# Kernel optimization log

Measured on AMD Instinct MI355X. Metric: run time of the kernel, lower is better.

The kernel has to match this reference:

```python
import jax, jax.numpy as jnp
import numpy as np

N, C, V, T, M = 4, 64, 25, 300, 2
H, HD = 8, 32
E = H * HD  # 256

def setup_inputs() -> dict:
    key = jax.random.key(0)
    ks = jax.random.split(key, 6)
    x = jax.random.normal(ks[0], (N, C, V, T, M), dtype=jnp.float32)
    w_qkv = jax.random.normal(ks[1], (C, 3 * E), dtype=jnp.float32) * (C ** -0.5)
    b_qkv = jnp.zeros((3 * E,), dtype=jnp.float32)
    w_merge = jax.random.normal(ks[2], (E, C), dtype=jnp.float32) * (E ** -0.5)
    b_merge = jnp.zeros((C,), dtype=jnp.float32)
    bias_table = jax.random.normal(ks[3], (2 * T - 1, HD), dtype=jnp.float32) * 0.02
    return {"x": x, "w_qkv": w_qkv, "b_qkv": b_qkv, "w_merge": w_merge,
            "b_merge": b_merge, "bias_table": bias_table}

def reference(x, w_qkv, b_qkv, w_merge, b_merge, bias_table):
    n, c, v, t, m = x.shape
    scale = E ** (-0.5)
    xp = jnp.transpose(x, (0, 4, 2, 3, 1))          # N M V T C
    qkv = xp @ w_qkv + b_qkv                         # N M V T 3E
    q, k, val = jnp.split(qkv, 3, axis=-1)
    def to_heads(z):
        z = z.reshape(n * m, v, t, H, HD)
        return jnp.transpose(z, (0, 1, 3, 2, 4))     # B V H T HD
    q, k, val = to_heads(q), to_heads(k), to_heads(val)
    scores = jnp.einsum('bvhid,bvhjd->bvhij', q, k) * scale
    rel = jnp.arange(t)
    idx = rel[:, None] - rel[None, :] + (t - 1)      # T T
    pos_bias = bias_table[idx]                       # T T HD
    rel_scores = jnp.einsum('bvhld,lrd->bvhlr', q, pos_bias)
    attn = jax.nn.softmax(scores + rel_scores, axis=-1)
    out = jnp.einsum('bvhij,bvhjd->bvhid', attn, val)  # B V H T HD
    out = jnp.transpose(out, (0, 1, 3, 2, 4)).reshape(n, m, v, t, E)
    out = out @ w_merge + b_merge                    # N M V T C
    return jnp.transpose(out, (0, 4, 2, 3, 1))       # N C V T M
```

## Files before the change

### kernel.cpp

```cpp
#include <hip/hip_runtime.h>
#include <cstdint>

#define NN 4
#define CC 64
#define VV 25
#define TT 300
#define MM 2
#define HH 8
#define HD 32
#define EE 256

typedef short bf16x8 __attribute__((ext_vector_type(8)));
typedef float f32x4 __attribute__((ext_vector_type(4)));
typedef float f32x2 __attribute__((ext_vector_type(2)));
typedef unsigned int u32x4 __attribute__((ext_vector_type(4)));

__device__ __forceinline__ unsigned short f2bf(float f) {
  union { float f; unsigned u; } x; x.f = f;
  unsigned r = x.u + 0x7FFF + ((x.u >> 16) & 1);
  return (unsigned short)(r >> 16);
}
__device__ __forceinline__ float bf2f(unsigned short s) {
  union { unsigned u; float f; } x; x.u = ((unsigned)s) << 16;
  return x.f;
}
__device__ __forceinline__ unsigned short truncbf(float f) {
  union { float f; unsigned u; } x; x.f = f;
  return (unsigned short)(x.u >> 16);
}
__device__ __forceinline__ float bperm(int byteaddr, float v) {
  return __int_as_float(__builtin_amdgcn_ds_bpermute(byteaddr, __float_as_int(v)));
}
__device__ __forceinline__ void unpack8(u32x4 a, u32x4 b, bf16x8& H8, bf16x8& L8) {
  union { unsigned u[4]; bf16x8 v; } H, L;
  H.u[0] = (a[1] & 0xFFFF0000u) | (a[0] >> 16);
  H.u[1] = (a[3] & 0xFFFF0000u) | (a[2] >> 16);
  H.u[2] = (b[1] & 0xFFFF0000u) | (b[0] >> 16);
  H.u[3] = (b[3] & 0xFFFF0000u) | (b[2] >> 16);
  L.u[0] = (a[1] << 16) | (a[0] & 0xFFFFu);
  L.u[1] = (a[3] << 16) | (a[2] & 0xFFFFu);
  L.u[2] = (b[1] << 16) | (b[0] & 0xFFFFu);
  L.u[3] = (b[3] << 16) | (b[2] & 0xFFFFu);
  H8 = H.v; L8 = L.v;
}

#define QKN 15360000
#define VTN 16384000
#define LOG2E 1.4426950408889634f

__global__ __launch_bounds__(256) void prep_kernel(
    const float* __restrict__ w_qkv, const float* __restrict__ w_merge,
    const float* __restrict__ bias_table,
    unsigned short* __restrict__ WqTh, unsigned short* __restrict__ WqTl,
    unsigned short* __restrict__ WhT, unsigned short* __restrict__ WlT,
    unsigned short* __restrict__ btPad)
{
  int i = blockIdx.x * 256 + threadIdx.x;
  if (i < 49152) {
    int c = i / 768, e = i % 768;
    float v = w_qkv[i];
    unsigned short hb = truncbf(v);
    WqTh[e * 64 + c] = hb; WqTl[e * 64 + c] = f2bf(v - bf2f(hb));
  } else if (i < 65536) {
    int j = i - 49152;
    int e = j >> 6, c = j & 63;
    float v = w_merge[j];
    unsigned short hb = truncbf(v);
    WhT[c * EE + e] = hb; WlT[c * EE + e] = f2bf(v - bf2f(hb));
  } else if (i < 65536 + 22528) {
    int j = i - 65536;
    int row = j >> 5, d = j & 31;
    int g = row - 20;
    float v = (g >= 0 && g < 2 * TT - 1) ? bias_table[g * 32 + d] : 0.f;
    btPad[j] = f2bf(v);
  }
}

__global__ __launch_bounds__(256, 3) void qkv_kernel(
    const float* __restrict__ x, const float* __restrict__ b_qkv,
    const unsigned short* __restrict__ WqTh, const unsigned short* __restrict__ WqTl,
    unsigned* __restrict__ Qp,
    unsigned short* __restrict__ Kh, unsigned short* __restrict__ Kl,
    unsigned short* __restrict__ Vt)
{
  __shared__ __align__(16) union {
    unsigned int a[64 * 68];
    unsigned short vtr[256 * 66];
  } sm;

  int blk = blockIdx.x;
  int tt = blk % 5; blk /= 5;
  int v25 = blk % 25; int b = blk / 25;
  int n = b >> 1, m = b & 1;
  int t0 = tt * 60;
  int tid = threadIdx.x;
  int w = tid >> 6, lane = tid & 63, quad = lane >> 4, c16 = lane & 15;

  for (int i = tid; i < 64 * 64; i += 256) {
    int c = i >> 6, t = i & 63;
    float val = 0.f;
    if (t < 60) val = x[((((size_t)n * CC + c) * VV + v25) * TT + (t0 + t)) * MM + m];
    union { float f; unsigned u; } xb; xb.f = val;
    unsigned hi16 = xb.u & 0xFFFF0000u;
    unsigned short lb = f2bf(val - __uint_as_float(hi16));
    sm.a[t * 68 + c] = hi16 | (unsigned)lb;
  }
  __syncthreads();

  bf16x8 ah[4][2], al[4][2];
  #pragma unroll
  for (int mt = 0; mt < 4; ++mt)
    #pragma unroll
    for (int kc = 0; kc < 2; ++kc) {
      const u32x4* p = (const u32x4*)&sm.a[(mt * 16 + c16) * 68 + kc * 32 + quad * 8];
      unpack8(p[0], p[1], ah[mt][kc], al[mt][kc]);
    }
  __syncthreads();

  size_t bv = (size_t)(b * VV + v25);
  int e0w = w * 192;
  for (int nt = 0; nt < 12; ++nt) {
    int ebase = e0w + nt * 16;
    int e = ebase + c16;
    bf16x8 bh[2], bl[2];
    #pragma unroll
    for (int kc = 0; kc < 2; ++kc) {
      bh[kc] = *(const bf16x8*)&WqTh[(size_t)e * 64 + kc * 32 + quad * 8];
      bl[kc] = *(const bf16x8*)&WqTl[(size_t)e * 64 + kc * 32 + quad * 8];
    }
    f32x4 acc[4];
    #pragma unroll
    for (int mt = 0; mt < 4; ++mt) {
      acc[mt] = (f32x4){0.f, 0.f, 0.f, 0.f};
      #pragma unroll
      for (int kc = 0; kc < 2; ++kc) {
        acc[mt] = __builtin_amdgcn_mfma_f32_16x16x32_bf16(ah[mt][kc], bh[kc], acc[mt], 0, 0, 0);
        acc[mt] = __builtin_amdgcn_mfma_f32_16x16x32_bf16(al[mt][kc], bh[kc], acc[mt], 0, 0, 0);
        acc[mt] = __builtin_amdgcn_mfma_f32_16x16x32_bf16(ah[mt][kc], bl[kc], acc[mt], 0, 0, 0);
      }
    }
    float bias = b_qkv[e];
    int which = ebase >> 8;
    if (which == 0) {
      int hh = (e >> 5) & 7, dd = e & 31;
      size_t rowb = (bv * HH + hh) * TT;
      #pragma unroll
      for (int mt = 0; mt < 4; ++mt)
        #pragma unroll
        for (int reg = 0; reg < 4; ++reg) {
          int lrow = mt * 16 + quad * 4 + reg;
          if (lrow < 60) {
            int t = t0 + lrow;
            float s = (acc[mt][reg] + bias) * LOG2E;
            union { float f; unsigned u; } sb; sb.f = s;
            unsigned hi16 = sb.u & 0xFFFF0000u;
            unsigned short lb2 = f2bf(s - __uint_as_float(hi16));
            Qp[(rowb + t) * HD + dd] = hi16 | (unsigned)lb2;
          }
        }
    } else if (which == 1) {
      int hh = (e >> 5) & 7, dd = e & 31;
      size_t rowb = (bv * HH + hh) * TT;
      #pragma unroll
      for (int mt = 0; mt < 4; ++mt)
        #pragma unroll
        for (int reg = 0; reg < 4; ++reg) {
          int lrow = mt * 16 + quad * 4 + reg;
          if (lrow < 60) {
            int t = t0 + lrow;
            float s = (acc[mt][reg] + bias) * 0.0625f;
            unsigned short hb = truncbf(s);
            size_t idx = (rowb + t) * HD + dd;
            Kh[idx] = hb; Kl[idx] = f2bf(s - bf2f(hb));
          }
        }
    } else {
      int ep = e - 512;
      #pragma unroll
      for (int mt = 0; mt < 4; ++mt)
        #pragma unroll
        for (int reg = 0; reg < 4; ++reg)
          sm.vtr[ep * 66 + mt * 16 + quad * 4 + reg] = f2bf(acc[mt][reg] + bias);
    }
  }
  __syncthreads();
  for (int i = tid; i < 256 * 30; i += 256) {
    int ep = i / 30, tc = (i % 30) * 2;
    int e = 512 + ep;
    int hh = (e >> 5) & 7, dd = e & 31;
    size_t idx = ((bv * HH + hh) * HD + dd) * 320 + t0 + tc;
    *(unsigned int*)&Vt[idx] = *(const unsigned int*)&sm.vtr[ep * 66 + tc];
  }
}

__global__ __launch_bounds__(256, 3) void attn17_kernel(
    const unsigned* __restrict__ Qp,
    const unsigned short* __restrict__ Kh, const unsigned short* __restrict__ Kl,
    const unsigned short* __restrict__ Vt, const unsigned short* __restrict__ btPad,
    unsigned short* __restrict__ Oh, unsigned short* __restrict__ Ol)
{
  __shared__ __align__(16) unsigned short sPh[2][128 * 72];

  int bid0 = blockIdx.x;
  int bid = (bid0 & 7) * 600 + (bid0 >> 3);
  int lt = bid % 3; int rest = bid / 3;
  int h = rest & 7; rest >>= 3;
  int v = rest % 25; int b = rest / 25;
  int l0 = lt * 128;
  int tid = threadIdx.x;
  int w = tid >> 6, lane = tid & 63, quad = lane >> 4, c16 = lane & 15;
  if (l0 + 32 * w >= TT) return;
  size_t tbase = ((size_t)(b * VV + v) * HH + h) * TT;
  size_t vbase = ((size_t)(b * VV + v) * HH + h) * HD;

  const unsigned short* Qp16 = (const unsigned short*)Qp;
  bf16x8 qh[2], qlw[2];
  #pragma unroll
  for (int mt = 0; mt < 2; ++mt) {
    size_t qo = (tbase + l0 + w * 32 + mt * 16 + c16) * HD + quad * 8;
    bf16x8 raw0 = *(const bf16x8*)&Qp16[qo * 2];
    bf16x8 raw1 = *(const bf16x8*)&Qp16[qo * 2 + 8];
    union { bf16x8 v; u32x4 u; } A, B;
    A.v = raw0; B.v = raw1;
    unpack8(A.u, B.u, qh[mt], qlw[mt]);
  }

  int srcaddr[4]; bool sel[4];
  #pragma unroll
  for (int reg = 0; reg < 4; ++reg) {
    srcaddr[reg] = 4 * (quad * 16 + ((15 + 4 * quad + reg - c16) & 15));
    sel[reg] = (4 * quad + reg) > c16;
  }

  f32x4 accO[2][2];
  #pragma unroll
  for (int mt = 0; mt < 2; ++mt)
    #pragma unroll
    for (int no = 0; no < 2; ++no)
      accO[mt][no] = (f32x4){0.f, 0.f, 0.f, 0.f};
  float psum[2][4] = {{0.f, 0.f, 0.f, 0.f}, {0.f, 0.f, 0.f, 0.f}};

  #pragma unroll
  for (int rt = 0; rt < 5; ++rt) {
    const int r0 = rt * 64;
    unsigned short* myP = &sPh[rt & 1][32 * w * 72];

    const unsigned short* kb = &Kh[(tbase + r0 + c16) * HD + quad * 8];
    const unsigned short* lb = &Kl[(tbase + r0 + c16) * HD + quad * 8];
    bf16x8 khv[4], klv[4];
    #pragma unroll
    for (int nt = 0; nt < 4; ++nt) {
      khv[nt] = *(const bf16x8*)&kb[nt * 16 * HD];
      klv[nt] = *(const bf16x8*)&lb[nt * 16 * HD];
    }
    bf16x8 vv[2][2];
    if (rt > 0) {
      int p0 = r0 - 64;
      #pragma unroll
      for (int kc = 0; kc < 2; ++kc)
        #pragma unroll
        for (int no = 0; no < 2; ++no)
          vv[kc][no] = *(const bf16x8*)&Vt[(vbase + no * 16 + c16) * 320 + p0 + kc * 32 + quad * 8];
    }
    const unsigned short* btb = &btPad[(size_t)(l0 + 256 + 32 * w - r0 + c16) * HD + quad * 8];
    bf16x8 bt6[6];
    #pragma unroll
    for (int j = 0; j < 6; ++j) bt6[j] = *(const bf16x8*)&btb[j * 16 * HD];

    #pragma unroll
    for (int mt = 0; mt < 2; ++mt) {
      float BA[4], BB[4], BC[4] = {0.f, 0.f, 0.f, 0.f};
      {
        f32x4 r = {0.f, 0.f, 0.f, 0.f};
        r = __builtin_amdgcn_mfma_f32_16x16x32_bf16(qh[mt], bt6[mt + 4], r, 0, 0, 0);
        f32x4 r2 = {0.f, 0.f, 0.f, 0.f};
        r2 = __builtin_amdgcn_mfma_f32_16x16x32_bf16(qh[mt], bt6[mt + 3], r2, 0, 0, 0);
        #pragma unroll
        for (int reg = 0; reg < 4; ++reg) BA[reg] = bperm(srcaddr[reg], r[reg]);
        #pragma unroll
        for (int reg = 0; reg < 4; ++reg) BB[reg] = bperm(srcaddr[reg], r2[reg]);
      }
      #pragma unroll
      for (int nt = 0; nt < 4; ++nt) {
        f32x4 sc = {0.f, 0.f, 0.f, 0.f};
        sc = __builtin_amdgcn_mfma_f32_16x16x32_bf16(qh[mt],  khv[nt], sc, 0, 0, 0);
        sc = __builtin_amdgcn_mfma_f32_16x16x32_bf16(qlw[mt], khv[nt], sc, 0, 0, 0);
        sc = __builtin_amdgcn_mfma_f32_16x16x32_bf16(qh[mt],  klv[nt], sc, 0, 0, 0);
        if (nt < 3) {
          f32x4 r = {0.f, 0.f, 0.f, 0.f};
          r = __builtin_amdgcn_mfma_f32_16x16x32_bf16(qh[mt], bt6[mt + 2 - nt], r, 0, 0, 0);
          #pragma unroll
          for (int reg = 0; reg < 4; ++reg) BC[reg] = bperm(srcaddr[reg], r[reg]);
        }

        bool bad = (r0 + nt * 16 + c16) >= TT;
        #pragma unroll
        for (int reg = 0; reg < 4; ++reg) {
          float ri = sel[reg] ? BA[reg] : BB[reg];
          float p = bad ? 0.f : __builtin_amdgcn_exp2f(sc[reg] + ri);
          psum[mt][reg] += p;
          myP[(mt * 16 + 4 * quad + reg) * 72 + nt * 16 + c16] = f2bf(p);
        }
        #pragma unroll
        for (int reg = 0; reg < 4; ++reg) { BA[reg] = BB[reg]; BB[reg] = BC[reg]; }
      }
    }

    if (rt > 0) {
      unsigned short* prevP = &sPh[(rt - 1) & 1][32 * w * 72];
      #pragma unroll
      for (int mt = 0; mt < 2; ++mt)
        #pragma unroll
        for (int kc = 0; kc < 2; ++kc) {
          bf16x8 pf = *(const bf16x8*)&prevP[(mt * 16 + c16) * 72 + kc * 32 + quad * 8];
          #pragma unroll
          for (int no = 0; no < 2; ++no)
            accO[mt][no] = __builtin_amdgcn_mfma_f32_16x16x32_bf16(pf, vv[kc][no], accO[mt][no], 0, 0, 0);
        }
    }
  }
  {
    int p0 = 4 * 64;
    unsigned short* prevP = &sPh[0][32 * w * 72];
    #pragma unroll
    for (int kc = 0; kc < 2; ++kc) {
      bf16x8 vfr[2];
      #pragma unroll
      for (int no = 0; no < 2; ++no)
        vfr[no] = *(const bf16x8*)&Vt[(vbase + no * 16 + c16) * 320 + p0 + kc * 32 + quad * 8];
      #pragma unroll
      for (int mt = 0; mt < 2; ++mt) {
        bf16x8 pf = *(const bf16x8*)&prevP[(mt * 16 + c16) * 72 + kc * 32 + quad * 8];
        #pragma unroll
        for (int no = 0; no < 2; ++no)
          accO[mt][no] = __builtin_amdgcn_mfma_f32_16x16x32_bf16(pf, vfr[no], accO[mt][no], 0, 0, 0);
      }
    }
  }

  #pragma unroll
  for (int mt = 0; mt < 2; ++mt)
    #pragma unroll
    for (int reg = 0; reg < 4; ++reg) {
      #pragma unroll
      for (int off = 1; off <= 8; off <<= 1)
        psum[mt][reg] += __shfl_xor(psum[mt][reg], off);
    }
  size_t obase = (size_t)(b * VV + v) * TT;
  #pragma unroll
  for (int mt = 0; mt < 2; ++mt)
    #pragma unroll
    for (int no = 0; no < 2; ++no)
      #pragma unroll
      for (int reg = 0; reg < 4; ++reg) {
        int gl = l0 + 32 * w + 16 * mt + 4 * quad + reg;
        if (gl < TT) {
          float o = accO[mt][no][reg] / psum[mt][reg];
          size_t oi = (obase + gl) * EE + h * HD + no * 16 + c16;
          unsigned short hb = truncbf(o);
          Oh[oi] = hb; Ol[oi] = f2bf(o - bf2f(hb));
        }
      }
}

__global__ __launch_bounds__(256, 4) void merge4_kernel(
    const unsigned short* __restrict__ Oh, const unsigned short* __restrict__ Ol,
    const unsigned short* __restrict__ WhT, const unsigned short* __restrict__ WlT,
    const float* __restrict__ b_merge, float* __restrict__ out)
{
  int blk = blockIdx.x;
  int tt = blk % 10; blk /= 10;
  int v = blk % 25; int nb = blk / 25;
  int tid = threadIdx.x;
  int w = tid >> 6, lane = tid & 63, quad = lane >> 4, c16 = lane & 15;
  int t0 = tt * 30;
  int cidx = w * 16 + c16;
  size_t obase0 = ((size_t)(nb * 2 + 0) * VV + v) * TT;
  size_t obase1 = ((size_t)(nb * 2 + 1) * VV + v) * TT;

  f32x4 acc[2][2];
  #pragma unroll
  for (int mm = 0; mm < 2; ++mm)
    #pragma unroll
    for (int mt = 0; mt < 2; ++mt)
      acc[mm][mt] = (f32x4){0.f, 0.f, 0.f, 0.f};

  for (int ks = 0; ks < 8; ++ks) {
    int eoff = ks * 32 + quad * 8;
    bf16x8 bh = *(const bf16x8*)&WhT[(size_t)cidx * EE + eoff];
    bf16x8 bl = *(const bf16x8*)&WlT[(size_t)cidx * EE + eoff];
    #pragma unroll
    for (int mm = 0; mm < 2; ++mm) {
      size_t ob = (mm == 0) ? obase0 : obase1;
      #pragma unroll
      for (int mt = 0; mt < 2; ++mt) {
        size_t ao = (ob + t0 + mt * 16 + c16) * EE + eoff;
        bf16x8 ahv = *(const bf16x8*)&Oh[ao];
        bf16x8 alv = *(const bf16x8*)&Ol[ao];
        acc[mm][mt] = __builtin_amdgcn_mfma_f32_16x16x32_bf16(ahv, bh, acc[mm][mt], 0, 0, 0);
        acc[mm][mt] = __builtin_amdgcn_mfma_f32_16x16x32_bf16(alv, bh, acc[mm][mt], 0, 0, 0);
        acc[mm][mt] = __builtin_amdgcn_mfma_f32_16x16x32_bf16(ahv, bl, acc[mm][mt], 0, 0, 0);
      }
    }
  }
  float bm = b_merge[cidx];
  size_t rowbase = ((size_t)nb * CC + cidx) * VV + v;
  #pragma unroll
  for (int mt = 0; mt < 2; ++mt)
    #pragma unroll
    for (int reg = 0; reg < 4; ++reg) {
      int lrow = mt * 16 + 4 * quad + reg;
      if (lrow < 30) {
        int t = t0 + lrow;
        f32x2 pr;
        pr[0] = acc[0][mt][reg] + bm;
        pr[1] = acc[1][mt][reg] + bm;
        *(f32x2*)&out[rowbase * TT * MM + (size_t)t * MM] = pr;
      }
    }
}

extern "C" void kernel_launch(void* const* d_in, const int* in_sizes, int n_in,
                              void* d_out, int out_size, void* d_ws, size_t ws_size,
                              hipStream_t stream) {
  const float* x          = (const float*)d_in[0];
  const float* w_qkv      = (const float*)d_in[1];
  const float* b_qkv      = (const float*)d_in[2];
  const float* w_merge    = (const float*)d_in[3];
  const float* b_merge    = (const float*)d_in[4];
  const float* bias_table = (const float*)d_in[5];
  float* out = (float*)d_out;
  unsigned short* ws16 = (unsigned short*)d_ws;
  unsigned* Qp = (unsigned*)ws16;
  unsigned short* Kh   = ws16 + (size_t)2 * QKN;
  unsigned short* Kl   = ws16 + (size_t)3 * QKN;
  unsigned short* Vt   = ws16 + (size_t)4 * QKN;
  unsigned short* Oh   = ws16 + (size_t)4 * QKN + VTN;
  unsigned short* Ol   = ws16 + (size_t)5 * QKN + VTN;
  unsigned short* base8 = ws16 + (size_t)6 * QKN + VTN;
  unsigned short* WhT  = base8;
  unsigned short* WlT  = base8 + 16384;
  unsigned short* WqTh = base8 + 32768;
  unsigned short* WqTl = base8 + 81920;
  unsigned short* btPad = base8 + 131072;

  prep_kernel<<<dim3(344), dim3(256), 0, stream>>>(w_qkv, w_merge, bias_table,
                                                   WqTh, WqTl, WhT, WlT, btPad);
  qkv_kernel<<<dim3(1000), dim3(256), 0, stream>>>(x, b_qkv, WqTh, WqTl,
                                                   Qp, Kh, Kl, Vt);
  attn17_kernel<<<dim3(4800), dim3(256), 0, stream>>>(Qp, Kh, Kl, Vt, btPad, Oh, Ol);
  merge4_kernel<<<dim3(1000), dim3(256), 0, stream>>>(Oh, Ol, WhT, WlT, b_merge, out);
}
```

Baseline: 296.0 us.

## Fuse attention and merge projection into one kernel looping over heads

The attention and merge kernels become one kernel. Each block now handles one (b, v, l-tile) and loops over all 8 heads. After each head it normalises the output, stages it in LDS as a hi/lo bf16 split, and accumulates that head's part of the merge GEMM in registers. This removes the Oh/Ol round-trip through global memory and one kernel launch. The cost is a grid cut from 4800 to 600 blocks, which reduces parallelism on a device with many CUs, and the final stores are scattered scalar writes.

```diff
diff --git a/kernel.cpp b/kernel.cpp
--- a/kernel.cpp
+++ b/kernel.cpp
@@ -193,37 +193,26 @@
   }
 }
 
-__global__ __launch_bounds__(256, 3) void attn17_kernel(
+__global__ __launch_bounds__(256, 3) void attn_merge_kernel(
     const unsigned* __restrict__ Qp,
     const unsigned short* __restrict__ Kh, const unsigned short* __restrict__ Kl,
     const unsigned short* __restrict__ Vt, const unsigned short* __restrict__ btPad,
-    unsigned short* __restrict__ Oh, unsigned short* __restrict__ Ol)
+    const unsigned short* __restrict__ WhT, const unsigned short* __restrict__ WlT,
+    const float* __restrict__ b_merge, float* __restrict__ out)
 {
   __shared__ __align__(16) unsigned short sPh[2][128 * 72];
+  __shared__ __align__(16) unsigned oLds[4 * 32 * 32];
 
   int bid0 = blockIdx.x;
-  int bid = (bid0 & 7) * 600 + (bid0 >> 3);
+  int bid = (bid0 & 7) * 75 + (bid0 >> 3);
   int lt = bid % 3; int rest = bid / 3;
-  int h = rest & 7; rest >>= 3;
   int v = rest % 25; int b = rest / 25;
   int l0 = lt * 128;
   int tid = threadIdx.x;
   int w = tid >> 6, lane = tid & 63, quad = lane >> 4, c16 = lane & 15;
   if (l0 + 32 * w >= TT) return;
-  size_t tbase = ((size_t)(b * VV + v) * HH + h) * TT;
-  size_t vbase = ((size_t)(b * VV + v) * HH + h) * HD;
 
   const unsigned short* Qp16 = (const unsigned short*)Qp;
-  bf16x8 qh[2], qlw[2];
-  #pragma unroll
-  for (int mt = 0; mt < 2; ++mt) {
-    size_t qo = (tbase + l0 + w * 32 + mt * 16 + c16) * HD + quad * 8;
-    bf16x8 raw0 = *(const bf16x8*)&Qp16[qo * 2];
-    bf16x8 raw1 = *(const bf16x8*)&Qp16[qo * 2 + 8];
-    union { bf16x8 v; u32x4 u; } A, B;
-    A.v = raw0; B.v = raw1;
-    unpack8(A.u, B.u, qh[mt], qlw[mt]);
-  }
 
   int srcaddr[4]; bool sel[4];
   #pragma unroll
@@ -232,192 +221,190 @@
     sel[reg] = (4 * quad + reg) > c16;
   }
 
-  f32x4 accO[2][2];
+  f32x4 oacc[2][4];
   #pragma unroll
   for (int mt = 0; mt < 2; ++mt)
     #pragma unroll
-    for (int no = 0; no < 2; ++no)
-      accO[mt][no] = (f32x4){0.f, 0.f, 0.f, 0.f};
-  float psum[2][4] = {{0.f, 0.f, 0.f, 0.f}, {0.f, 0.f, 0.f, 0.f}};
-
+    for (int ct = 0; ct < 4; ++ct)
+      oacc[mt][ct] = (f32x4){0.f, 0.f, 0.f, 0.f};
+
+  unsigned* oL = &oLds[w * 1024];
+
+  for (int h = 0; h < 8; ++h) {
+    size_t tbase = ((size_t)(b * VV + v) * HH + h) * TT;
+    size_t vbase = ((size_t)(b * VV + v) * HH + h) * HD;
+
+    bf16x8 qh[2], qlw[2];
+    #pragma unroll
+    for (int mt = 0; mt < 2; ++mt) {
+      size_t qo = (tbase + l0 + w * 32 + mt * 16 + c16) * HD + quad * 8;
+      bf16x8 raw0 = *(const bf16x8*)&Qp16[qo * 2];
+      bf16x8 raw1 = *(const bf16x8*)&Qp16[qo * 2 + 8];
+      union { bf16x8 v; u32x4 u; } A, B;
+      A.v = raw0; B.v = raw1;
+      unpack8(A.u, B.u, qh[mt], qlw[mt]);
+    }
+
+    f32x4 accO[2][2];
+    #pragma unroll
+    for (int mt = 0; mt < 2; ++mt)
+      #pragma unroll
+      for (int no = 0; no < 2; ++no)
+        accO[mt][no] = (f32x4){0.f, 0.f, 0.f, 0.f};
+    float psum[2][4] = {{0.f, 0.f, 0.f, 0.f}, {0.f, 0.f, 0.f, 0.f}};
+
+    #pragma unroll
+    for (int rt = 0; rt < 5; ++rt) {
+      const int r0 = rt * 64;
+      unsigned short* myP = &sPh[rt & 1][32 * w * 72];
+
+      const unsigned short* kb = &Kh[(tbase + r0 + c16) * HD + quad * 8];
+      const unsigned short* lb = &Kl[(tbase + r0 + c16) * HD + quad * 8];
+      bf16x8 khv[4], klv[4];
+      #pragma unroll
+      for (int nt = 0; nt < 4; ++nt) {
+        khv[nt] = *(const bf16x8*)&kb[nt * 16 * HD];
+        klv[nt] = *(const bf16x8*)&lb[nt * 16 * HD];
+      }
+      bf16x8 vv[2][2];
+      if (rt > 0) {
+        int p0 = r0 - 64;
+        #pragma unroll
+        for (int kc = 0; kc < 2; ++kc)
+          #pragma unroll
+          for (int no = 0; no < 2; ++no)
+            vv[kc][no] = *(const bf16x8*)&Vt[(vbase + no * 16 + c16) * 320 + p0 + kc * 32 + quad * 8];
+      }
+      const unsigned short* btb = &btPad[(size_t)(l0 + 256 + 32 * w - r0 + c16) * HD + quad * 8];
+      bf16x8 bt6[6];
+      #pragma unroll
+      for (int j = 0; j < 6; ++j) bt6[j] = *(const bf16x8*)&btb[j * 16 * HD];
+
+      #pragma unroll
+      for (int mt = 0; mt < 2; ++mt) {
+        float BA[4], BB[4], BC[4] = {0.f, 0.f, 0.f, 0.f};
+        {
+          f32x4 r = {0.f, 0.f, 0.f, 0.f};
+          r = __builtin_amdgcn_mfma_f32_16x16x32_bf16(qh[mt], bt6[mt + 4], r, 0, 0, 0);
+          f32x4 r2 = {0.f, 0.f, 0.f, 0.f};
+          r2 = __builtin_amdgcn_mfma_f32_16x16x32_bf16(qh[mt], bt6[mt + 3], r2, 0, 0, 0);
+          #pragma unroll
+          for (int reg = 0; reg < 4; ++reg) BA[reg] = bperm(srcaddr[reg], r[reg]);
+          #pragma unroll
+          for (int reg = 0; reg < 4; ++reg) BB[reg] = bperm(srcaddr[reg], r2[reg]);
+        }
+        #pragma unroll
+        for (int nt = 0; nt < 4; ++nt) {
+          f32x4 sc = {0.f, 0.f, 0.f, 0.f};
+          sc = __builtin_amdgcn_mfma_f32_16x16x32_bf16(qh[mt],  khv[nt], sc, 0, 0, 0);
+          sc = __builtin_amdgcn_mfma_f32_16x16x32_bf16(qlw[mt], khv[nt], sc, 0, 0, 0);
+          sc = __builtin_amdgcn_mfma_f32_16x16x32_bf16(qh[mt],  klv[nt], sc, 0, 0, 0);
+          if (nt < 3) {
+            f32x4 r = {0.f, 0.f, 0.f, 0.f};
+            r = __builtin_amdgcn_mfma_f32_16x16x32_bf16(qh[mt], bt6[mt + 2 - nt], r, 0, 0, 0);
+            #pragma unroll
+            for (int reg = 0; reg < 4; ++reg) BC[reg] = bperm(srcaddr[reg], r[reg]);
+          }
+
+          bool bad = (r0 + nt * 16 + c16) >= TT;
+          #pragma unroll
+          for (int reg = 0; reg < 4; ++reg) {
+            float ri = sel[reg] ? BA[reg] : BB[reg];
+            float p = bad ? 0.f : __builtin_amdgcn_exp2f(sc[reg] + ri);
+            psum[mt][reg] += p;
+            myP[(mt * 16 + 4 * quad + reg) * 72 + nt * 16 + c16] = f2bf(p);
+          }
+          #pragma unroll
+          for (int reg = 0; reg < 4; ++reg) { BA[reg] = BB[reg]; BB[reg] = BC[reg]; }
+        }
+      }
+
+      if (rt > 0) {
+        unsigned short* prevP = &sPh[(rt - 1) & 1][32 * w * 72];
+        #pragma unroll
+        for (int mt = 0; mt < 2; ++mt)
+          #pragma unroll
+          for (int kc = 0; kc < 2; ++kc) {
+            bf16x8 pf = *(const bf16x8*)&prevP[(mt * 16 + c16) * 72 + kc * 32 + quad * 8];
+            #pragma unroll
+            for (int no = 0; no < 2; ++no)
+              accO[mt][no] = __builtin_amdgcn_mfma_f32_16x16x32_bf16(pf, vv[kc][no], accO[mt][no], 0, 0, 0);
+          }
+      }
+    }
+    {
+      int p0 = 4 * 64;
+      unsigned short* prevP = &sPh[0][32 * w * 72];
+      #pragma unroll
+      for (int kc = 0; kc < 2; ++kc) {
+        bf16x8 vfr[2];
+        #pragma unroll
+        for (int no = 0; no < 2; ++no)
+          vfr[no] = *(const bf16x8*)&Vt[(vbase + no * 16 + c16) * 320 + p0 + kc * 32 + quad * 8];
+        #pragma unroll
+        for (int mt = 0; mt < 2; ++mt) {
+          bf16x8 pf = *(const bf16x8*)&prevP[(mt * 16 + c16) * 72 + kc * 32 + quad * 8];
+          #pragma unroll
+          for (int no = 0; no < 2; ++no)
+            accO[mt][no] = __builtin_amdgcn_mfma_f32_16x16x32_bf16(pf, vfr[no], accO[mt][no], 0, 0, 0);
+        }
+      }
+    }
+
+    #pragma unroll
+    for (int mt = 0; mt < 2; ++mt)
+      #pragma unroll
+      for (int reg = 0; reg < 4; ++reg) {
+        #pragma unroll
+        for (int off = 1; off <= 8; off <<= 1)
+          psum[mt][reg] += __shfl_xor(psum[mt][reg], off);
+      }
+    #pragma unroll
+    for (int mt = 0; mt < 2; ++mt)
+      #pragma unroll
+      for (int no = 0; no < 2; ++no)
+        #pragma unroll
+        for (int reg = 0; reg < 4; ++reg) {
+          float o = accO[mt][no][reg] / psum[mt][reg];
+          unsigned short hb = truncbf(o);
+          unsigned short lb = f2bf(o - bf2f(hb));
+          oL[(mt * 16 + 4 * quad + reg) * 32 + no * 16 + c16] = ((unsigned)hb << 16) | (unsigned)lb;
+        }
+
+    #pragma unroll
+    for (int mt = 0; mt < 2; ++mt) {
+      const u32x4* p = (const u32x4*)&oL[(mt * 16 + c16) * 32 + quad * 8];
+      u32x4 a0 = p[0], a1 = p[1];
+      bf16x8 oh8, ol8;
+      unpack8(a0, a1, oh8, ol8);
+      #pragma unroll
+      for (int ct = 0; ct < 4; ++ct) {
+        bf16x8 bh = *(const bf16x8*)&WhT[(size_t)(ct * 16 + c16) * EE + h * 32 + quad * 8];
+        bf16x8 bl = *(const bf16x8*)&WlT[(size_t)(ct * 16 + c16) * EE + h * 32 + quad * 8];
+        oacc[mt][ct] = __builtin_amdgcn_mfma_f32_16x16x32_bf16(oh8, bh, oacc[mt][ct], 0, 0, 0);
+        oacc[mt][ct] = __builtin_amdgcn_mfma_f32_16x16x32_bf16(ol8, bh, oacc[mt][ct], 0, 0, 0);
+        oacc[mt][ct] = __builtin_amdgcn_mfma_f32_16x16x32_bf16(oh8, bl, oacc[mt][ct], 0, 0, 0);
+      }
+    }
+  }
+
+  int n = b >> 1, m = b & 1;
+  float bmv[4];
   #pragma unroll
-  for (int rt = 0; rt < 5; ++rt) {
-    const int r0 = rt * 64;
-    unsigned short* myP = &sPh[rt & 1][32 * w * 72];
-
-    const unsigned short* kb = &Kh[(tbase + r0 + c16) * HD + quad * 8];
-    const unsigned short* lb = &Kl[(tbase + r0 + c16) * HD + quad * 8];
-    bf16x8 khv[4], klv[4];
-    #pragma unroll
-    for (int nt = 0; nt < 4; ++nt) {
-      khv[nt] = *(const bf16x8*)&kb[nt * 16 * HD];
-      klv[nt] = *(const bf16x8*)&lb[nt * 16 * HD];
-    }
-    bf16x8 vv[2][2];
-    if (rt > 0) {
-      int p0 = r0 - 64;
-      #pragma unroll
-      for (int kc = 0; kc < 2; ++kc)
-        #pragma unroll
-        for (int no = 0; no < 2; ++no)
-          vv[kc][no] = *(const bf16x8*)&Vt[(vbase + no * 16 + c16) * 320 + p0 + kc * 32 + quad * 8];
-    }
-    const unsigned short* btb = &btPad[(size_t)(l0 + 256 + 32 * w - r0 + c16) * HD + quad * 8];
-    bf16x8 bt6[6];
-    #pragma unroll
-    for (int j = 0; j < 6; ++j) bt6[j] = *(const bf16x8*)&btb[j * 16 * HD];
-
-    #pragma unroll
-    for (int mt = 0; mt < 2; ++mt) {
-      float BA[4], BB[4], BC[4] = {0.f, 0.f, 0.f, 0.f};
-      {
-        f32x4 r = {0.f, 0.f, 0.f, 0.f};
-        r = __builtin_amdgcn_mfma_f32_16x16x32_bf16(qh[mt], bt6[mt + 4], r, 0, 0, 0);
-        f32x4 r2 = {0.f, 0.f, 0.f, 0.f};
-        r2 = __builtin_amdgcn_mfma_f32_16x16x32_bf16(qh[mt], bt6[mt + 3], r2, 0, 0, 0);
-        #pragma unroll
-        for (int reg = 0; reg < 4; ++reg) BA[reg] = bperm(srcaddr[reg], r[reg]);
-        #pragma unroll
-        for (int reg = 0; reg < 4; ++reg) BB[reg] = bperm(srcaddr[reg], r2[reg]);
-      }
-      #pragma unroll
-      for (int nt = 0; nt < 4; ++nt) {
-        f32x4 sc = {0.f, 0.f, 0.f, 0.f};
-        sc = __builtin_amdgcn_mfma_f32_16x16x32_bf16(qh[mt],  khv[nt], sc, 0, 0, 0);
-        sc = __builtin_amdgcn_mfma_f32_16x16x32_bf16(qlw[mt], khv[nt], sc, 0, 0, 0);
-        sc = __builtin_amdgcn_mfma_f32_16x16x32_bf16(qh[mt],  klv[nt], sc, 0, 0, 0);
-        if (nt < 3) {
-          f32x4 r = {0.f, 0.f, 0.f, 0.f};
-          r = __builtin_amdgcn_mfma_f32_16x16x32_bf16(qh[mt], bt6[mt + 2 - nt], r, 0, 0, 0);
-          #pragma unroll
-          for (int reg = 0; reg < 4; ++reg) BC[reg] = bperm(srcaddr[reg], r[reg]);
-        }
-
-        bool bad = (r0 + nt * 16 + c16) >= TT;
-        #pragma unroll
-        for (int reg = 0; reg < 4; ++reg) {
-          float ri = sel[reg] ? BA[reg] : BB[reg];
-          float p = bad ? 0.f : __builtin_amdgcn_exp2f(sc[reg] + ri);
-          psum[mt][reg] += p;
-          myP[(mt * 16 + 4 * quad + reg) * 72 + nt * 16 + c16] = f2bf(p);
-        }
-        #pragma unroll
-        for (int reg = 0; reg < 4; ++reg) { BA[reg] = BB[reg]; BB[reg] = BC[reg]; }
-      }
-    }
-
-    if (rt > 0) {
-      unsigned short* prevP = &sPh[(rt - 1) & 1][32 * w * 72];
-      #pragma unroll
-      for (int mt = 0; mt < 2; ++mt)
-        #pragma unroll
-        for (int kc = 0; kc < 2; ++kc) {
-          bf16x8 pf = *(const bf16x8*)&prevP[(mt * 16 + c16) * 72 + kc * 32 + quad * 8];
-          #pragma unroll
-          for (int no = 0; no < 2; ++no)
-            accO[mt][no] = __builtin_amdgcn_mfma_f32_16x16x32_bf16(pf, vv[kc][no], accO[mt][no], 0, 0, 0);
-        }
-    }
-  }
-  {
-    int p0 = 4 * 64;
-    unsigned short* prevP = &sPh[0][32 * w * 72];
-    #pragma unroll
-    for (int kc = 0; kc < 2; ++kc) {
-      bf16x8 vfr[2];
-      #pragma unroll
-      for (int no = 0; no < 2; ++no)
-        vfr[no] = *(const bf16x8*)&Vt[(vbase + no * 16 + c16) * 320 + p0 + kc * 32 + quad * 8];
-      #pragma unroll
-      for (int mt = 0; mt < 2; ++mt) {
-        bf16x8 pf = *(const bf16x8*)&prevP[(mt * 16 + c16) * 72 + kc * 32 + quad * 8];
-        #pragma unroll
-        for (int no = 0; no < 2; ++no)
-          accO[mt][no] = __builtin_amdgcn_mfma_f32_16x16x32_bf16(pf, vfr[no], accO[mt][no], 0, 0, 0);
-      }
-    }
-  }
-
+  for (int ct = 0; ct < 4; ++ct) bmv[ct] = b_merge[ct * 16 + c16];
   #pragma unroll
   for (int mt = 0; mt < 2; ++mt)
     #pragma unroll
-    for (int reg = 0; reg < 4; ++reg) {
-      #pragma unroll
-      for (int off = 1; off <= 8; off <<= 1)
-        psum[mt][reg] += __shfl_xor(psum[mt][reg], off);
-    }
-  size_t obase = (size_t)(b * VV + v) * TT;
-  #pragma unroll
-  for (int mt = 0; mt < 2; ++mt)
-    #pragma unroll
-    for (int no = 0; no < 2; ++no)
+    for (int ct = 0; ct < 4; ++ct)
       #pragma unroll
       for (int reg = 0; reg < 4; ++reg) {
-        int gl = l0 + 32 * w + 16 * mt + 4 * quad + reg;
+        int gl = l0 + 32 * w + mt * 16 + 4 * quad + reg;
         if (gl < TT) {
-          float o = accO[mt][no][reg] / psum[mt][reg];
-          size_t oi = (obase + gl) * EE + h * HD + no * 16 + c16;
-          unsigned short hb = truncbf(o);
-          Oh[oi] = hb; Ol[oi] = f2bf(o - bf2f(hb));
-        }
-      }
-}
-
-__global__ __launch_bounds__(256, 4) void merge4_kernel(
-    const unsigned short* __restrict__ Oh, const unsigned short* __restrict__ Ol,
-    const unsigned short* __restrict__ WhT, const unsigned short* __restrict__ WlT,
-    const float* __restrict__ b_merge, float* __restrict__ out)
-{
-  int blk = blockIdx.x;
-  int tt = blk % 10; blk /= 10;
-  int v = blk % 25; int nb = blk / 25;
-  int tid = threadIdx.x;
-  int w = tid >> 6, lane = tid & 63, quad = lane >> 4, c16 = lane & 15;
-  int t0 = tt * 30;
-  int cidx = w * 16 + c16;
-  size_t obase0 = ((size_t)(nb * 2 + 0) * VV + v) * TT;
-  size_t obase1 = ((size_t)(nb * 2 + 1) * VV + v) * TT;
-
-  f32x4 acc[2][2];
-  #pragma unroll
-  for (int mm = 0; mm < 2; ++mm)
-    #pragma unroll
-    for (int mt = 0; mt < 2; ++mt)
-      acc[mm][mt] = (f32x4){0.f, 0.f, 0.f, 0.f};
-
-  for (int ks = 0; ks < 8; ++ks) {
-    int eoff = ks * 32 + quad * 8;
-    bf16x8 bh = *(const bf16x8*)&WhT[(size_t)cidx * EE + eoff];
-    bf16x8 bl = *(const bf16x8*)&WlT[(size_t)cidx * EE + eoff];
-    #pragma unroll
-    for (int mm = 0; mm < 2; ++mm) {
-      size_t ob = (mm == 0) ? obase0 : obase1;
-      #pragma unroll
-      for (int mt = 0; mt < 2; ++mt) {
-        size_t ao = (ob + t0 + mt * 16 + c16) * EE + eoff;
-        bf16x8 ahv = *(const bf16x8*)&Oh[ao];
-        bf16x8 alv = *(const bf16x8*)&Ol[ao];
-        acc[mm][mt] = __builtin_amdgcn_mfma_f32_16x16x32_bf16(ahv, bh, acc[mm][mt], 0, 0, 0);
-        acc[mm][mt] = __builtin_amdgcn_mfma_f32_16x16x32_bf16(alv, bh, acc[mm][mt], 0, 0, 0);
-        acc[mm][mt] = __builtin_amdgcn_mfma_f32_16x16x32_bf16(ahv, bl, acc[mm][mt], 0, 0, 0);
-      }
-    }
-  }
-  float bm = b_merge[cidx];
-  size_t rowbase = ((size_t)nb * CC + cidx) * VV + v;
-  #pragma unroll
-  for (int mt = 0; mt < 2; ++mt)
-    #pragma unroll
-    for (int reg = 0; reg < 4; ++reg) {
-      int lrow = mt * 16 + 4 * quad + reg;
-      if (lrow < 30) {
-        int t = t0 + lrow;
-        f32x2 pr;
-        pr[0] = acc[0][mt][reg] + bm;
-        pr[1] = acc[1][mt][reg] + bm;
-        *(f32x2*)&out[rowbase * TT * MM + (size_t)t * MM] = pr;
-      }
-    }
+          int c = ct * 16 + c16;
+          out[(((size_t)n * CC + c) * VV + v) * TT * MM + (size_t)gl * MM + m]
+              = oacc[mt][ct][reg] + bmv[ct];
+        }
+      }
 }
 
 extern "C" void kernel_launch(void* const* d_in, const int* in_sizes, int n_in,
@@ -435,8 +422,6 @@
   unsigned short* Kh   = ws16 + (size_t)2 * QKN;
   unsigned short* Kl   = ws16 + (size_t)3 * QKN;
   unsigned short* Vt   = ws16 + (size_t)4 * QKN;
-  unsigned short* Oh   = ws16 + (size_t)4 * QKN + VTN;
-  unsigned short* Ol   = ws16 + (size_t)5 * QKN + VTN;
   unsigned short* base8 = ws16 + (size_t)6 * QKN + VTN;
   unsigned short* WhT  = base8;
   unsigned short* WlT  = base8 + 16384;
@@ -448,6 +433,6 @@
                                                    WqTh, WqTl, WhT, WlT, btPad);
   qkv_kernel<<<dim3(1000), dim3(256), 0, stream>>>(x, b_qkv, WqTh, WqTl,
                                                    Qp, Kh, Kl, Vt);
-  attn17_kernel<<<dim3(4800), dim3(256), 0, stream>>>(Qp, Kh, Kl, Vt, btPad, Oh, Ol);
-  merge4_kernel<<<dim3(1000), dim3(256), 0, stream>>>(Oh, Ol, WhT, WlT, b_merge, out);
-}
+  attn_merge_kernel<<<dim3(600), dim3(256), 0, stream>>>(Qp, Kh, Kl, Vt, btPad,
+                                                         WhT, WlT, b_merge, out);
+}
```

New measurement: 394.0 us. 33.1% more time.
